# Optimization experiments

Hardware: AMD Instinct MI355X
Metric: run time of the kernel (lower is better)

## Reference

```python
import jax, jax.numpy as jnp
import numpy as np

B, T, D, H, L, FF, V = 32, 64, 512, 8, 4, 2048, 128
HD = D // H
TEMP = 0.1
SCALE_BASE = 16.0
NEG = -1e9


def setup_inputs() -> dict:
    key = jax.random.key(0)
    cnt = [0]
    def nk():
        cnt[0] += 1
        return jax.random.fold_in(key, cnt[0])
    def rn(shape, s=0.02):
        return jax.random.normal(nk(), shape, dtype=jnp.float32) * s
    inp = {
        "target_tensor": jax.random.randint(nk(), (B, T), 0, V),
        "mol_encoding": jax.random.normal(nk(), (B, D), dtype=jnp.float32),
        "emb": rn((V, D), 1.0),
        "sa_in_w": rn((L, 3 * D, D)), "sa_in_b": jnp.zeros((L, 3 * D), jnp.float32),
        "sa_out_w": rn((L, D, D)), "sa_out_b": jnp.zeros((L, D), jnp.float32),
        "ca_in_w": rn((L, 3 * D, D)), "ca_in_b": jnp.zeros((L, 3 * D), jnp.float32),
        "ca_out_w": rn((L, D, D)), "ca_out_b": jnp.zeros((L, D), jnp.float32),
        "ff_w1": rn((L, FF, D)), "ff_b1": jnp.zeros((L, FF), jnp.float32),
        "ff_w2": rn((L, D, FF)), "ff_b2": jnp.zeros((L, D), jnp.float32),
        "n1_g": jnp.ones((L, D), jnp.float32), "n1_b": jnp.zeros((L, D), jnp.float32),
        "n2_g": jnp.ones((L, D), jnp.float32), "n2_b": jnp.zeros((L, D), jnp.float32),
        "n3_g": jnp.ones((L, D), jnp.float32), "n3_b": jnp.zeros((L, D), jnp.float32),
        "fn_g": jnp.ones((D,), jnp.float32), "fn_b": jnp.zeros((D,), jnp.float32),
        "out_w1": rn((2 * D, D)), "out_b1": jnp.zeros((2 * D,), jnp.float32),
        "out_w2": rn((1024, 2 * D)), "out_b2": jnp.zeros((1024,), jnp.float32),
        "out_w3": rn((V, 1024)), "out_b3": jnp.zeros((V,), jnp.float32),
    }
    return inp


def _ln(x, g, b, eps=1e-5):
    mu = x.mean(-1, keepdims=True)
    var = ((x - mu) ** 2).mean(-1, keepdims=True)
    return (x - mu) * jax.lax.rsqrt(var + eps) * g + b


def _xpos(x):
    # x: [B, T, D]; XPOS rotary with scale_base=16, downscale=False
    t, d = x.shape[1], x.shape[2]
    half = d // 2
    sv = (jnp.arange(0, d, 2, dtype=jnp.float32) + 0.4 * d) / (1.4 * d)      # [half]
    pos = jnp.arange(t, dtype=jnp.float32)
    scale = sv[None, :] ** (pos / SCALE_BASE)[:, None]                       # [t, half]
    inv_freq = 1.0 / (10000.0 ** (jnp.arange(half, dtype=jnp.float32) / half))
    ang = pos[:, None] * inv_freq[None, :]                                   # [t, half]
    sin = jnp.repeat(jnp.sin(ang) * scale, 2, axis=-1)                       # duplicate_interleave
    cos = jnp.repeat(jnp.cos(ang) * scale, 2, axis=-1)
    x1, x2 = x[..., ::2], x[..., 1::2]
    rot = jnp.stack((-x2, x1), axis=-1).reshape(x.shape)                     # rotate_every_two
    return x * cos + rot * sin


def _mha(q_in, k_in, v_in, in_w, in_b, out_w, out_b, mask):
    wq, wk, wv = jnp.split(in_w, 3, axis=0)
    bq, bk, bv = jnp.split(in_b, 3, axis=0)
    Bq, Tq = q_in.shape[0], q_in.shape[1]
    q = (q_in @ wq.T + bq).reshape(Bq, Tq, H, HD)
    k = (k_in @ wk.T + bk).reshape(Bq, -1, H, HD)
    v = (v_in @ wv.T + bv).reshape(Bq, -1, H, HD)
    scores = jnp.einsum('bqhd,bkhd->bhqk', q, k) / np.float32(np.sqrt(HD))
    if mask is not None:
        scores = jnp.where(mask, NEG, scores)
    p = jax.nn.softmax(scores, axis=-1)
    o = jnp.einsum('bhqk,bkhd->bqhd', p, v).reshape(Bq, Tq, D)
    return o @ out_w.T + out_b


def reference(target_tensor, mol_encoding, emb, sa_in_w, sa_in_b, sa_out_w, sa_out_b,
              ca_in_w, ca_in_b, ca_out_w, ca_out_b, ff_w1, ff_b1, ff_w2, ff_b2,
              n1_g, n1_b, n2_g, n2_b, n3_g, n3_b, fn_g, fn_b,
              out_w1, out_b1, out_w2, out_b2, out_w3, out_b3):
    memory = mol_encoding[:, None, :]                      # [B, 1, D]
    causal = jnp.triu(jnp.ones((T, T), bool), 1)
    samp_key = jax.random.key(1)

    def logits_at(pred, t):
        x = _xpos(emb[pred])                               # [B, T, D]
        mask = causal[None, None] | (pred == 0)[:, None, None, :]
        for i in range(L):
            a = _mha(x, x, x, sa_in_w[i], sa_in_b[i], sa_out_w[i], sa_out_b[i], mask)
            x = _ln(x + a, n1_g[i], n1_b[i])
            c = _mha(x, memory, memory, ca_in_w[i], ca_in_b[i], ca_out_w[i], ca_out_b[i], None)
            x = _ln(x + c, n2_g[i], n2_b[i])
            f = jax.nn.silu(x @ ff_w1[i].T + ff_b1[i]) @ ff_w2[i].T + ff_b2[i]
            x = _ln(x + f, n3_g[i], n3_b[i])
        x = _ln(x, fn_g, fn_b)
        h = jnp.take(x, t - 1, axis=1)                     # [B, D]
        h = jax.nn.gelu(h @ out_w1.T + out_b1, approximate=False)
        h = jax.nn.gelu(h @ out_w2.T + out_b2, approximate=False)
        return h @ out_w3.T + out_b3                       # [B, V]

    def step(pred, t):
        logits = logits_at(pred, t)
        lp = jax.nn.log_softmax(logits / TEMP, axis=-1)
        u = jax.random.uniform(jax.random.fold_in(samp_key, t), lp.shape)
        g = -jnp.log(-jnp.log(u + 1e-9) + 1e-9)
        tok = jnp.argmax(lp + g, axis=-1).astype(jnp.int32)
        return pred.at[:, t].set(tok), logits

    pred0 = jnp.zeros((B, T), jnp.int32).at[:, 0].set(1)
    pred, _ = jax.lax.scan(jax.checkpoint(step), pred0, jnp.arange(1, T))
    return pred
```

## Files before the change

kernel.cpp:

```cpp
#include <hip/hip_runtime.h>
#include <stdint.h>
#include <stddef.h>

#define BB 32
#define TT 64
#define DD 512
#define HH 8
#define HDIM 64
#define LL 4
#define FFD 2048
#define VV 128

#define NBLK 256
#define NTHR 512

__host__ __device__ inline uint32_t rotl32(uint32_t v, int n){ return (v << n) | (v >> (32 - n)); }

__host__ __device__ inline void tf2x32(uint32_t k0, uint32_t k1, uint32_t x0, uint32_t x1,
                                       uint32_t* o0, uint32_t* o1){
  uint32_t ks2 = k0 ^ k1 ^ 0x1BD11BDAu;
  x0 += k0; x1 += k1;
  x0 += x1; x1 = rotl32(x1,13); x1 ^= x0;
  x0 += x1; x1 = rotl32(x1,15); x1 ^= x0;
  x0 += x1; x1 = rotl32(x1,26); x1 ^= x0;
  x0 += x1; x1 = rotl32(x1, 6); x1 ^= x0;
  x0 += k1; x1 += ks2 + 1u;
  x0 += x1; x1 = rotl32(x1,17); x1 ^= x0;
  x0 += x1; x1 = rotl32(x1,29); x1 ^= x0;
  x0 += x1; x1 = rotl32(x1,16); x1 ^= x0;
  x0 += x1; x1 = rotl32(x1,24); x1 ^= x0;
  x0 += ks2; x1 += k0 + 2u;
  x0 += x1; x1 = rotl32(x1,13); x1 ^= x0;
  x0 += x1; x1 = rotl32(x1,15); x1 ^= x0;
  x0 += x1; x1 = rotl32(x1,26); x1 ^= x0;
  x0 += x1; x1 = rotl32(x1, 6); x1 ^= x0;
  x0 += k0; x1 += k1 + 3u;
  x0 += x1; x1 = rotl32(x1,17); x1 ^= x0;
  x0 += x1; x1 = rotl32(x1,29); x1 ^= x0;
  x0 += x1; x1 = rotl32(x1,16); x1 ^= x0;
  x0 += x1; x1 = rotl32(x1,24); x1 ^= x0;
  x0 += k1; x1 += ks2 + 4u;
  x0 += x1; x1 = rotl32(x1,13); x1 ^= x0;
  x0 += x1; x1 = rotl32(x1,15); x1 ^= x0;
  x0 += x1; x1 = rotl32(x1,26); x1 ^= x0;
  x0 += x1; x1 = rotl32(x1, 6); x1 ^= x0;
  x0 += ks2; x1 += k0 + 5u;
  *o0 = x0; *o1 = x1;
}

__device__ inline float dot_f4(const float* __restrict__ a, const float* __restrict__ w, int K){
  float acc = 0.f;
  const float4* a4 = (const float4*)a;
  const float4* w4 = (const float4*)w;
  int K4 = K >> 2;
  for (int k = 0; k < K4; ++k){
    float4 av = a4[k], wv = w4[k];
    acc = fmaf(av.x, wv.x, acc);
    acc = fmaf(av.y, wv.y, acc);
    acc = fmaf(av.z, wv.z, acc);
    acc = fmaf(av.w, wv.w, acc);
  }
  return acc;
}

__device__ inline float block_ln(float v, float g, float bb, float* red){
  __syncthreads();
  float s = v;
  #pragma unroll
  for (int off = 32; off; off >>= 1) s += __shfl_xor(s, off);
  if ((threadIdx.x & 63) == 0) red[threadIdx.x >> 6] = s;
  __syncthreads();
  float mu = (red[0]+red[1]+red[2]+red[3]+red[4]+red[5]+red[6]+red[7]) * (1.0f/512.0f);
  float dv = v - mu;
  float sq = dv * dv;
  #pragma unroll
  for (int off = 32; off; off >>= 1) sq += __shfl_xor(sq, off);
  __syncthreads();
  if ((threadIdx.x & 63) == 0) red[threadIdx.x >> 6] = sq;
  __syncthreads();
  float var = (red[0]+red[1]+red[2]+red[3]+red[4]+red[5]+red[6]+red[7]) * (1.0f/512.0f);
  return dv * (1.0f / sqrtf(var + 1e-5f)) * g + bb;
}

__device__ inline float row_reduce(float v, int wid, int j, float* wred){
  #pragma unroll
  for (int off = 32; off; off >>= 1) v += __shfl_xor(v, off);
  if ((threadIdx.x & 63) == 0) wred[wid] = v;
  __syncthreads();
  float r = wred[2*j] + wred[2*j+1];
  __syncthreads();
  return r;
}

__device__ __forceinline__ void gbar(unsigned* bar, int g){
  __syncthreads();
  if (threadIdx.x == 0){
    unsigned* cnt = bar + g*64;
    unsigned* gen = bar + g*64 + 16;
    __builtin_amdgcn_fence(__ATOMIC_RELEASE, "agent");
    unsigned old = __hip_atomic_load(gen, __ATOMIC_RELAXED, __HIP_MEMORY_SCOPE_AGENT);
    if (__hip_atomic_fetch_add(cnt, 1u, __ATOMIC_RELAXED, __HIP_MEMORY_SCOPE_AGENT) == 31u){
      __hip_atomic_store(cnt, 0u, __ATOMIC_RELAXED, __HIP_MEMORY_SCOPE_AGENT);
      __hip_atomic_fetch_add(gen, 1u, __ATOMIC_RELEASE, __HIP_MEMORY_SCOPE_AGENT);
    } else {
      while (__hip_atomic_load(gen, __ATOMIC_RELAXED, __HIP_MEMORY_SCOPE_AGENT) == old)
        __builtin_amdgcn_s_sleep(1);
    }
    __builtin_amdgcn_fence(__ATOMIC_ACQUIRE, "agent");
  }
  __syncthreads();
}

__global__ void k_tables(float* __restrict__ cosb, float* __restrict__ sinb){
  int tid = blockIdx.x * blockDim.x + threadIdx.x;
  int p = tid >> 8, i = tid & 255;
  float sv = (2.0f * (float)i + 204.8f) / 716.8f;
  float scale = powf(sv, (float)p / 16.0f);
  float invf = 1.0f / powf(10000.0f, (float)i / 256.0f);
  float ang = (float)p * invf;
  cosb[tid] = cosf(ang) * scale;
  sinb[tid] = sinf(ang) * scale;
}

__global__ void k_ca1(const float* __restrict__ mol, const float* __restrict__ w,
                      const float* __restrict__ bias, float* __restrict__ tmp){
  int tid = blockIdx.x * blockDim.x + threadIdx.x;
  int l = tid >> 14; int r = tid & 16383; int b = r >> 9; int d = r & 511;
  const float* wr = w + (size_t)l*3*DD*DD + (size_t)(2*DD + d)*DD;
  tmp[tid] = bias[l*3*DD + 2*DD + d] + dot_f4(mol + (size_t)b*DD, wr, DD);
}

__global__ void k_ca2(const float* __restrict__ tmp, const float* __restrict__ w,
                      const float* __restrict__ bias, float* __restrict__ cac){
  int tid = blockIdx.x * blockDim.x + threadIdx.x;
  int l = tid >> 14; int r = tid & 16383; int b = r >> 9; int d = r & 511;
  const float* wr = w + (size_t)l*DD*DD + (size_t)d*DD;
  cac[tid] = bias[l*DD + d] + dot_f4(tmp + ((size_t)l*BB + b)*DD, wr, DD);
}

__global__ void k_binit(unsigned* __restrict__ bar, int* __restrict__ pred){
  int tid = threadIdx.x;
  bar[tid] = 0u;
  pred[tid]        = ((tid & (TT-1)) == 0) ? 1 : 0;
  pred[tid + 1024] = (((tid + 1024) & (TT-1)) == 0) ? 1 : 0;
}

__global__ void k_pack32(const float* __restrict__ in, float* __restrict__ out,
                         int N, int K, int total){
  int tid = blockIdx.x * blockDim.x + threadIdx.x;
  if (tid >= total) return;
  int S = N * K;
  int l = tid / S, r = tid - l*S;
  int k32 = r / (32*N);
  int r2 = r - k32*32*N;
  int n = r2 >> 5, ku = r2 & 31;
  out[tid] = in[(size_t)l*S + (size_t)n*K + k32*32 + ku];
}

#define CELL4(WARR, KOFF)                                                     \
  _Pragma("unroll")                                                           \
  for (int q = 0; q < 8; ++q){                                                \
    float4 w = WARR[q];                                                       \
    const int kk = (KOFF) + q*4;                                              \
    float4 xa = *(const float4*)&sxp[0*512 + kk];                             \
    float4 xb = *(const float4*)&sxp[1*512 + kk];                             \
    float4 xc = *(const float4*)&sxp[2*512 + kk];                             \
    float4 xd = *(const float4*)&sxp[3*512 + kk];                             \
    a0=fmaf(w.x,xa.x,a0); a0=fmaf(w.y,xa.y,a0); a0=fmaf(w.z,xa.z,a0); a0=fmaf(w.w,xa.w,a0); \
    a1=fmaf(w.x,xb.x,a1); a1=fmaf(w.y,xb.y,a1); a1=fmaf(w.z,xb.z,a1); a1=fmaf(w.w,xb.w,a1); \
    a2=fmaf(w.x,xc.x,a2); a2=fmaf(w.y,xc.y,a2); a2=fmaf(w.z,xc.z,a2); a2=fmaf(w.w,xc.w,a2); \
    a3=fmaf(w.x,xd.x,a3); a3=fmaf(w.y,xd.y,a3); a3=fmaf(w.z,xd.z,a3); a3=fmaf(w.w,xd.w,a3); \
  }

struct KParams {
  const float *emb, *sab, *sob, *f1b, *f2b;
  const float *g1,*b1,*g2,*b2,*g3,*b3,*fg,*fb;
  const float *o1b,*o2b,*o3w,*o3b;
  const float *cosb,*sinb,*cac;
  const float *sawP,*sowP,*f1wP,*f2wP,*o1wP,*o2wP;
  float *kc,*vc,*xl,*qb,*at,*ao,*x2,*fo,*h1,*xf,*hh1,*hh2,*ps3;
  int *pred;
  unsigned *bar;
};

__global__ __launch_bounds__(NTHR) void k_persist(KParams P){
  const int bid = blockIdx.x, tid = threadIdx.x;
  const int g = bid & 7;
  const int m = bid >> 3;
  const int wid = tid >> 6, lane = tid & 63;
  __shared__ __align__(16) float smem[8704];

  for (int t = 1; t < TT; ++t){
    const int pp = t - 1;

    for (int l = 0; l < LL; ++l){
      {
        float* sx   = smem;
        float* part = smem + 2048;
        float* srow = smem + 4096;
        const int j = tid >> 7, d4 = (tid & 127) * 4;
        const int rb = g*4 + j;
        if (l == 0){
          int tok = P.pred[rb*TT + pp];
          #pragma unroll
          for (int e = d4; e < d4 + 4; e += 2){
            int i = e >> 1;
            float c = P.cosb[pp*256 + i], s = P.sinb[pp*256 + i];
            float e0 = P.emb[(size_t)tok*DD + e];
            float e1 = P.emb[(size_t)tok*DD + e + 1];
            sx[j*512 + e]     = fmaf(e0, c, -(e1*s));
            sx[j*512 + e + 1] = fmaf(e1, c, e0*s);
          }
        } else {
          if (tid < 4){
            float a = 0.f, bq = 0.f;
            const float* pr = P.ps3 + (size_t)(g*4 + tid)*64;
            for (int s = 0; s < 32; ++s){ a += pr[s*2]; bq += pr[s*2+1]; }
            float mu = a * (1.0f/512.0f);
            float var = bq * (1.0f/512.0f) - mu*mu;
            srow[tid*2]   = mu;
            srow[tid*2+1] = 1.0f / sqrtf(var + 1e-5f);
          }
          __syncthreads();
          float mu = srow[j*2], rs = srow[j*2+1];
          float4 xv = *(const float4*)&P.x2[(size_t)rb*DD + d4];
          float4 fv = *(const float4*)&P.fo[(size_t)rb*DD + d4];
          const float* g3r = P.g3 + (size_t)(l-1)*DD;
          const float* b3r = P.b3 + (size_t)(l-1)*DD;
          float yv[4] = {xv.x+fv.x, xv.y+fv.y, xv.z+fv.z, xv.w+fv.w};
          #pragma unroll
          for (int i = 0; i < 4; ++i)
            sx[j*512 + d4 + i] = (yv[i]-mu)*rs*g3r[d4+i] + b3r[d4+i];
        }
        __syncthreads();
        if (m == 0){
          float4 v = *(float4*)&sx[j*512 + d4];
          *(float4*)&P.xl[(size_t)rb*DD + d4] = v;
        }
        if (m < 24){
          const int n0 = m*64;
          const float4* wb0 = (const float4*)P.sawP + ((size_t)l*16 + wid*2)*(1536*8)
                            + (size_t)(n0 + lane)*8;
          const float4* wb1 = wb0 + 1536*8;
          float4 w0[8], w1[8];
          #pragma unroll
          for (int q = 0; q < 8; ++q) w0[q] = wb0[q];
          #pragma unroll
          for (int q = 0; q < 8; ++q) w1[q] = wb1[q];
          float a0=0.f,a1=0.f,a2=0.f,a3=0.f;
          const float* sxp = sx;
          const int kb = wid*64;
          CELL4(w0, kb);
          CELL4(w1, kb + 32);
          part[(wid*4+0)*64 + lane] = a0;
          part[(wid*4+1)*64 + lane] = a1;
          part[(wid*4+2)*64 + lane] = a2;
          part[(wid*4+3)*64 + lane] = a3;
          __syncthreads();
          if (tid < 256){
            int jr = tid >> 6, nl = tid & 63;
            int n = n0 + nl, rb2 = g*4 + jr;
            float s = P.sab[l*1536 + n];
            #pragma unroll
            for (int w = 0; w < 8; ++w) s += part[(w*4+jr)*64 + nl];
            if (n < DD){
              P.qb[(size_t)rb2*DD + n] = s;
            } else if (n < 2*DD){
              int h = (n - DD) >> 6, hd = (n - DD) & 63;
              P.kc[((((size_t)l*BB + rb2)*HH + h)*TT + pp)*HDIM + hd] = s;
            } else {
              int h = (n - 2*DD) >> 6, hd = (n - 2*DD) & 63;
              P.vc[((((size_t)l*BB + rb2)*HH + h)*TT + pp)*HDIM + hd] = s;
            }
          }
        }
      }
      gbar(P.bar, g);

      {
        int bl = m >> 3, h = m & 7, rb = g*4 + bl;
        float* qs = smem; float* ps = smem + 64;
        if (tid < 64) qs[tid] = P.qb[(size_t)rb*DD + h*HDIM + tid];
        __syncthreads();
        if (tid < 64){
          const float* kb = P.kc + (((size_t)l*BB + rb)*HH + h)*TT*HDIM;
          float s = -INFINITY;
          if (lane <= pp && P.pred[rb*TT + lane] != 0){
            const float* kr = kb + lane*HDIM;
            float acc = 0.f;
            #pragma unroll
            for (int k2 = 0; k2 < HDIM; ++k2) acc = fmaf(qs[k2], kr[k2], acc);
            s = acc * 0.125f;
          }
          float mx = s;
          #pragma unroll
          for (int off = 32; off; off >>= 1) mx = fmaxf(mx, __shfl_xor(mx, off));
          float e = (s == -INFINITY) ? 0.f : expf(s - mx);
          float sum = e;
          #pragma unroll
          for (int off = 32; off; off >>= 1) sum += __shfl_xor(sum, off);
          ps[lane] = e / sum;
          const float* vb = P.vc + (((size_t)l*BB + rb)*HH + h)*TT*HDIM;
          float o = 0.f;
          int jj = 0;
          for (; jj + 8 <= t; jj += 8){
            float vv[8];
            #pragma unroll
            for (int u = 0; u < 8; ++u) vv[u] = vb[(jj+u)*HDIM + lane];
            #pragma unroll
            for (int u = 0; u < 8; ++u) o = fmaf(ps[jj+u], vv[u], o);
          }
          for (; jj <= pp; ++jj) o = fmaf(ps[jj], vb[jj*HDIM + lane], o);
          P.at[(size_t)rb*DD + h*HDIM + lane] = o;
        }
      }
      gbar(P.bar, g);

      {
        float* ats  = smem;
        float* part = smem + 2048;
        const int j = tid >> 7, d4 = (tid & 127) * 4;
        *(float4*)&ats[j*512 + d4] = *(const float4*)&P.at[(size_t)(g*4+j)*DD + d4];
        __syncthreads();
        const int n0 = m*16;
        const int jb = lane >> 4, nc = lane & 15;
        const float4* wb0 = (const float4*)P.sowP + ((size_t)l*16 + wid*2)*(512*8)
                          + (size_t)(n0 + nc)*8;
        const float4* wb1 = wb0 + 512*8;
        float4 w0[8], w1[8];
        #pragma unroll
        for (int q = 0; q < 8; ++q) w0[q] = wb0[q];
        #pragma unroll
        for (int q = 0; q < 8; ++q) w1[q] = wb1[q];
        float acc = 0.f;
        const int kb = wid*64;
        #pragma unroll
        for (int q = 0; q < 8; ++q){
          float4 w = w0[q];
          float4 xa = *(const float4*)&ats[jb*512 + kb + q*4];
          acc=fmaf(w.x,xa.x,acc); acc=fmaf(w.y,xa.y,acc); acc=fmaf(w.z,xa.z,acc); acc=fmaf(w.w,xa.w,acc);
        }
        #pragma unroll
        for (int q = 0; q < 8; ++q){
          float4 w = w1[q];
          float4 xa = *(const float4*)&ats[jb*512 + kb + 32 + q*4];
          acc=fmaf(w.x,xa.x,acc); acc=fmaf(w.y,xa.y,acc); acc=fmaf(w.z,xa.z,acc); acc=fmaf(w.w,xa.w,acc);
        }
        part[wid*64 + lane] = acc;
        __syncthreads();
        if (tid < 64){
          int jb2 = tid >> 4, nc2 = tid & 15, n = n0 + nc2;
          float s = P.sob[l*DD + n];
          #pragma unroll
          for (int w = 0; w < 8; ++w) s += part[w*64 + jb2*16 + nc2];
          P.ao[(size_t)(g*4+jb2)*DD + n] = s;
        }
      }
      gbar(P.bar, g);

      {
        float* sx2  = smem;
        float* part = smem + 2048;
        float* wred = smem + 4096;
        const int j = tid >> 7, d4 = (tid & 127) * 4;
        const int rb = g*4 + j;
        float4 xlv = *(const float4*)&P.xl[(size_t)rb*DD + d4];
        float4 aov = *(const float4*)&P.ao[(size_t)rb*DD + d4];
        float y[4] = {xlv.x+aov.x, xlv.y+aov.y, xlv.z+aov.z, xlv.w+aov.w};
        float s = ((y[0]+y[1])+y[2])+y[3];
        float mu = row_reduce(s, wid, j, wred) * (1.0f/512.0f);
        float dv[4], sq = 0.f;
        #pragma unroll
        for (int i = 0; i < 4; ++i){ dv[i] = y[i]-mu; sq += dv[i]*dv[i]; }
        float rs = 1.0f / sqrtf(row_reduce(sq, wid, j, wred) * (1.0f/512.0f) + 1e-5f);
        float z[4];
        #pragma unroll
        for (int i = 0; i < 4; ++i){
          int d = d4 + i;
          z[i] = dv[i]*rs*P.g1[l*DD+d] + P.b1[l*DD+d] + P.cac[((size_t)l*BB + rb)*DD + d];
        }
        float s2 = ((z[0]+z[1])+z[2])+z[3];
        float mu2 = row_reduce(s2, wid, j, wred) * (1.0f/512.0f);
        float dz[4], sq2 = 0.f;
        #pragma unroll
        for (int i = 0; i < 4; ++i){ dz[i] = z[i]-mu2; sq2 += dz[i]*dz[i]; }
        float rs2 = 1.0f / sqrtf(row_reduce(sq2, wid, j, wred) * (1.0f/512.0f) + 1e-5f);
        float x2v[4];
        #pragma unroll
        for (int i = 0; i < 4; ++i){
          int d = d4 + i;
          x2v[i] = dz[i]*rs2*P.g2[l*DD+d] + P.b2[l*DD+d];
          sx2[j*512 + d] = x2v[i];
        }
        if (m == 0) *(float4*)&P.x2[(size_t)rb*DD + d4] = make_float4(x2v[0],x2v[1],x2v[2],x2v[3]);
        __syncthreads();
        const int n0 = m*64;
        const float4* wb0 = (const float4*)P.f1wP + ((size_t)l*16 + wid*2)*(2048*8)
                          + (size_t)(n0 + lane)*8;
        const float4* wb1 = wb0 + 2048*8;
        float4 w0[8], w1[8];
        #pragma unroll
        for (int q = 0; q < 8; ++q) w0[q] = wb0[q];
        #pragma unroll
        for (int q = 0; q < 8; ++q) w1[q] = wb1[q];
        float a0=0.f,a1=0.f,a2=0.f,a3=0.f;
        const float* sxp = sx2;
        const int kb = wid*64;
        CELL4(w0, kb);
        CELL4(w1, kb + 32);
        part[(wid*4+0)*64 + lane] = a0;
        part[(wid*4+1)*64 + lane] = a1;
        part[(wid*4+2)*64 + lane] = a2;
        part[(wid*4+3)*64 + lane] = a3;
        __syncthreads();
        if (tid < 256){
          int jr = tid >> 6, nl = tid & 63;
          int n = n0 + nl;
          float v = P.f1b[l*FFD + n];
          #pragma unroll
          for (int w = 0; w < 8; ++w) v += part[(w*4+jr)*64 + nl];
          P.h1[(size_t)(g*4+jr)*FFD + n] = v / (1.0f + expf(-v));
        }
      }
      gbar(P.bar, g);

      {
        float* sh1  = smem;
        float* part = smem + 8192;
        #pragma unroll
        for (int q = 0; q < 4; ++q){
          int fi = tid + q*512;
          int j = fi >> 9, c4 = fi & 511;
          *(float4*)&sh1[j*2048 + c4*4] = *(const float4*)&P.h1[(size_t)(g*4+j)*FFD + c4*4];
        }
        __syncthreads();
        const int n0 = m*16;
        const int jb = lane >> 4, nc = lane & 15;
        const float4* base = (const float4*)P.f2wP + ((size_t)l*64 + wid*8)*(512*8)
                           + (size_t)(n0 + nc)*8;
        float acc = 0.f;
        #pragma unroll
        for (int cc = 0; cc < 4; ++cc){
          const float4* b0 = base + (size_t)(cc*2)*(512*8);
          const float4* b1 = b0 + 512*8;
          float4 w0[8], w1[8];
          #pragma unroll
          for (int q = 0; q < 8; ++q) w0[q] = b0[q];
          #pragma unroll
          for (int q = 0; q < 8; ++q) w1[q] = b1[q];
          const int kb = wid*256 + cc*64;
          #pragma unroll
          for (int q = 0; q < 8; ++q){
            float4 w = w0[q];
            float4 xa = *(const float4*)&sh1[jb*2048 + kb + q*4];
            acc=fmaf(w.x,xa.x,acc); acc=fmaf(w.y,xa.y,acc); acc=fmaf(w.z,xa.z,acc); acc=fmaf(w.w,xa.w,acc);
          }
          #pragma unroll
          for (int q = 0; q < 8; ++q){
            float4 w = w1[q];
            float4 xa = *(const float4*)&sh1[jb*2048 + kb + 32 + q*4];
            acc=fmaf(w.x,xa.x,acc); acc=fmaf(w.y,xa.y,acc); acc=fmaf(w.z,xa.z,acc); acc=fmaf(w.w,xa.w,acc);
          }
        }
        part[wid*64 + lane] = acc;
        __syncthreads();
        if (tid < 64){
          int jb2 = tid >> 4, nc2 = tid & 15, n = n0 + nc2;
          int rb2 = g*4 + jb2;
          float val = P.f2b[l*DD + n];
          #pragma unroll
          for (int w = 0; w < 8; ++w) val += part[w*64 + jb2*16 + nc2];
          P.fo[(size_t)rb2*DD + n] = val;
          float y = P.x2[(size_t)rb2*DD + n] + val;
          float s1 = y, sq = y*y;
          #pragma unroll
          for (int off = 1; off < 16; off <<= 1){
            s1 += __shfl_xor(s1, off);
            sq += __shfl_xor(sq, off);
          }
          if (nc2 == 0){
            P.ps3[(size_t)(rb2*32 + m)*2]     = s1;
            P.ps3[(size_t)(rb2*32 + m)*2 + 1] = sq;
          }
        }
      }
      gbar(P.bar, g);
    }

    if (m < 4){
      int rb = g*4 + m, d = tid;
      float y = P.x2[(size_t)rb*DD + d] + P.fo[(size_t)rb*DD + d];
      float xv = block_ln(y, P.g3[3*DD + d], P.b3[3*DD + d], smem);
      float o  = block_ln(xv, P.fg[d], P.fb[d], smem);
      P.xf[(size_t)rb*DD + d] = o;
    }
    gbar(P.bar, g);

    {
      float* sxf  = smem;
      float* part = smem + 2048;
      const int j = tid >> 7, d4 = (tid & 127) * 4;
      *(float4*)&sxf[j*512 + d4] = *(const float4*)&P.xf[(size_t)(g*4+j)*DD + d4];
      __syncthreads();
      const int n0 = m*32;
      const int jh = lane >> 5, nc = lane & 31;
      const float4* wb0 = (const float4*)P.o1wP + (size_t)(wid*2)*(1024*8)
                        + (size_t)(n0 + nc)*8;
      const float4* wb1 = wb0 + 1024*8;
      float4 w0[8], w1[8];
      #pragma unroll
      for (int q = 0; q < 8; ++q) w0[q] = wb0[q];
      #pragma unroll
      for (int q = 0; q < 8; ++q) w1[q] = wb1[q];
      float ac0 = 0.f, ac1 = 0.f;
      const int kb = wid*64;
      #pragma unroll
      for (int q = 0; q < 8; ++q){
        float4 w = w0[q];
        float4 xa = *(const float4*)&sxf[jh*512 + kb + q*4];
        float4 xb = *(const float4*)&sxf[(jh+2)*512 + kb + q*4];
        ac0=fmaf(w.x,xa.x,ac0); ac0=fmaf(w.y,xa.y,ac0); ac0=fmaf(w.z,xa.z,ac0); ac0=fmaf(w.w,xa.w,ac0);
        ac1=fmaf(w.x,xb.x,ac1); ac1=fmaf(w.y,xb.y,ac1); ac1=fmaf(w.z,xb.z,ac1); ac1=fmaf(w.w,xb.w,ac1);
      }
      #pragma unroll
      for (int q = 0; q < 8; ++q){
        float4 w = w1[q];
        float4 xa = *(const float4*)&sxf[jh*512 + kb + 32 + q*4];
        float4 xb = *(const float4*)&sxf[(jh+2)*512 + kb + 32 + q*4];
        ac0=fmaf(w.x,xa.x,ac0); ac0=fmaf(w.y,xa.y,ac0); ac0=fmaf(w.z,xa.z,ac0); ac0=fmaf(w.w,xa.w,ac0);
        ac1=fmaf(w.x,xb.x,ac1); ac1=fmaf(w.y,xb.y,ac1); ac1=fmaf(w.z,xb.z,ac1); ac1=fmaf(w.w,xb.w,ac1);
      }
      part[(wid*2+0)*64 + lane] = ac0;
      part[(wid*2+1)*64 + lane] = ac1;
      __syncthreads();
      if (tid < 128){
        int row = tid >> 5, nc2 = tid & 31;
        int r = row >> 1, jh2 = row & 1;
        float s = P.o1b[n0 + nc2];
        #pragma unroll
        for (int w = 0; w < 8; ++w) s += part[(w*2+r)*64 + jh2*32 + nc2];
        float a = s;
        P.hh1[(size_t)(g*4+row)*1024 + n0 + nc2] = 0.5f * a * (1.0f + erff(a / 1.41421356237309504880f));
      }
    }
    gbar(P.bar, g);

    {
      float* sh   = smem;
      float* part = smem + 4096;
      #pragma unroll
      for (int q = 0; q < 2; ++q){
        int fi = tid + q*512;
        int j = fi >> 8, c4 = fi & 255;
        *(float4*)&sh[j*1024 + c4*4] = *(const float4*)&P.hh1[(size_t)(g*4+j)*1024 + c4*4];
      }
      __syncthreads();
      const int n0 = m*32;
      const int jh = lane >> 5, nc = lane & 31;
      const float4* base = (const float4*)P.o2wP + (size_t)(wid*4)*(1024*8)
                         + (size_t)(n0 + nc)*8;
      float ac0 = 0.f, ac1 = 0.f;
      #pragma unroll
      for (int cc = 0; cc < 2; ++cc){
        const float4* b0 = base + (size_t)(cc*2)*(1024*8);
        const float4* b1 = b0 + 1024*8;
        float4 w0[8], w1[8];
        #pragma unroll
        for (int q = 0; q < 8; ++q) w0[q] = b0[q];
        #pragma unroll
        for (int q = 0; q < 8; ++q) w1[q] = b1[q];
        const int kb = wid*128 + cc*64;
        #pragma unroll
        for (int q = 0; q < 8; ++q){
          float4 w = w0[q];
          float4 xa = *(const float4*)&sh[jh*1024 + kb + q*4];
          float4 xb = *(const float4*)&sh[(jh+2)*1024 + kb + q*4];
          ac0=fmaf(w.x,xa.x,ac0); ac0=fmaf(w.y,xa.y,ac0); ac0=fmaf(w.z,xa.z,ac0); ac0=fmaf(w.w,xa.w,ac0);
          ac1=fmaf(w.x,xb.x,ac1); ac1=fmaf(w.y,xb.y,ac1); ac1=fmaf(w.z,xb.z,ac1); ac1=fmaf(w.w,xb.w,ac1);
        }
        #pragma unroll
        for (int q = 0; q < 8; ++q){
          float4 w = w1[q];
          float4 xa = *(const float4*)&sh[jh*1024 + kb + 32 + q*4];
          float4 xb = *(const float4*)&sh[(jh+2)*1024 + kb + 32 + q*4];
          ac0=fmaf(w.x,xa.x,ac0); ac0=fmaf(w.y,xa.y,ac0); ac0=fmaf(w.z,xa.z,ac0); ac0=fmaf(w.w,xa.w,ac0);
          ac1=fmaf(w.x,xb.x,ac1); ac1=fmaf(w.y,xb.y,ac1); ac1=fmaf(w.z,xb.z,ac1); ac1=fmaf(w.w,xb.w,ac1);
        }
      }
      part[(wid*2+0)*64 + lane] = ac0;
      part[(wid*2+1)*64 + lane] = ac1;
      __syncthreads();
      if (tid < 128){
        int row = tid >> 5, nc2 = tid & 31;
        int r = row >> 1, jh2 = row & 1;
        float s = P.o2b[n0 + nc2];
        #pragma unroll
        for (int w = 0; w < 8; ++w) s += part[(w*2+r)*64 + jh2*32 + nc2];
        float a = s;
        P.hh2[(size_t)(g*4+row)*1024 + n0 + nc2] = 0.5f * a * (1.0f + erff(a / 1.41421356237309504880f));
      }
    }
    gbar(P.bar, g);

    if (m < 4){
      int rb = g*4 + m, v = tid;
      float* hrow = smem;
      float* red  = smem + 1024;
      int*   redi = (int*)(smem + 1032);
      for (int k = tid; k < 1024; k += NTHR) hrow[k] = P.hh2[(size_t)rb*1024 + k];
      __syncthreads();
      float sv = 0.f;
      if (tid < 128){
        float acc = P.o3b[v] + dot_f4(hrow, P.o3w + (size_t)v*1024, 1024);
        sv = acc / 0.1f;
      }
      float mx = (tid < 128) ? sv : -INFINITY;
      #pragma unroll
      for (int off = 32; off; off >>= 1) mx = fmaxf(mx, __shfl_xor(mx, off));
      __syncthreads();
      if (tid < 128 && (tid & 63) == 0) red[tid >> 6] = mx;
      __syncthreads();
      mx = fmaxf(red[0], red[1]);
      float e = (tid < 128) ? expf(sv - mx) : 0.f;
      float sum = e;
      #pragma unroll
      for (int off = 32; off; off >>= 1) sum += __shfl_xor(sum, off);
      __syncthreads();
      if (tid < 128 && (tid & 63) == 0) red[tid >> 6] = sum;
      __syncthreads();
      sum = red[0] + red[1];
      float bv = -INFINITY; int bi = 0x7fffffff;
      if (tid < 128){
        float lp = (sv - mx) - logf(sum);
        uint32_t kk0, kk1, o0, o1;
        tf2x32(0u, 1u, 0u, (uint32_t)t, &kk0, &kk1);
        tf2x32(kk0, kk1, 0u, (uint32_t)(rb*VV + v), &o0, &o1);
        uint32_t bits = o0 ^ o1;
        float u = __uint_as_float((bits >> 9) | 0x3F800000u) - 1.0f;
        float gg = -logf(-logf(u + 1e-9f) + 1e-9f);
        bv = lp + gg; bi = v;
      }
      #pragma unroll
      for (int off = 32; off; off >>= 1){
        float ov = __shfl_xor(bv, off);
        int   oi = __shfl_xor(bi, off);
        if (ov > bv || (ov == bv && oi < bi)){ bv = ov; bi = oi; }
      }
      __syncthreads();
      if (tid < 128 && (tid & 63) == 0){ red[tid >> 6] = bv; redi[tid >> 6] = bi; }
      __syncthreads();
      if (tid == 0){
        float v0 = red[0], v1 = red[1]; int i0 = redi[0], i1 = redi[1];
        P.pred[rb*TT + t] = (v1 > v0 || (v1 == v0 && i1 < i0)) ? i1 : i0;
      }
    }
    gbar(P.bar, g);
  }
}

extern "C" void kernel_launch(void* const* d_in, const int* in_sizes, int n_in,
                              void* d_out, int out_size, void* d_ws, size_t ws_size,
                              hipStream_t stream){
  (void)in_sizes; (void)n_in; (void)out_size; (void)ws_size;
  const float* mol      = (const float*)d_in[1];
  const float* sa_in_w  = (const float*)d_in[3];
  const float* sa_out_w = (const float*)d_in[5];
  const float* ca_in_w  = (const float*)d_in[7];
  const float* ca_in_b  = (const float*)d_in[8];
  const float* ca_out_w = (const float*)d_in[9];
  const float* ca_out_b = (const float*)d_in[10];
  const float* ff_w1    = (const float*)d_in[11];
  const float* ff_w2    = (const float*)d_in[13];
  const float* out_w1   = (const float*)d_in[23];
  const float* out_w2   = (const float*)d_in[25];

  KParams P;
  P.emb = (const float*)d_in[2];
  P.sab = (const float*)d_in[4];
  P.sob = (const float*)d_in[6];
  P.f1b = (const float*)d_in[12];
  P.f2b = (const float*)d_in[14];
  P.g1  = (const float*)d_in[15];
  P.b1  = (const float*)d_in[16];
  P.g2  = (const float*)d_in[17];
  P.b2  = (const float*)d_in[18];
  P.g3  = (const float*)d_in[19];
  P.b3  = (const float*)d_in[20];
  P.fg  = (const float*)d_in[21];
  P.fb  = (const float*)d_in[22];
  P.o1b = (const float*)d_in[24];
  P.o2b = (const float*)d_in[26];
  P.o3w = (const float*)d_in[27];
  P.o3b = (const float*)d_in[28];

  unsigned* bar = (unsigned*)d_ws;
  float* ws = (float*)d_ws + 1024;
  float* cosb   = ws;
  float* sinb   = cosb + 16384;
  float* ca_tmp = sinb + 16384;
  float* cac    = ca_tmp + 65536;
  float* kc     = cac + 65536;
  float* vc     = kc + 4194304;
  float* xl     = vc + 4194304;
  float* qb     = xl + 16384;
  float* at     = qb + 16384;
  float* ao     = at + 16384;
  float* x2     = ao + 16384;
  float* fo     = x2 + 16384;
  float* h1     = fo + 16384;
  float* xf     = h1 + 65536;
  float* hh1    = xf + 16384;
  float* hh2    = hh1 + 32768;
  float* ps3    = hh2 + 32768;
  float* sawP   = ps3 + 2048;
  float* sowP   = sawP + 3145728;
  float* f1wP   = sowP + 1048576;
  float* f2wP   = f1wP + 4194304;
  float* o1wP   = f2wP + 4194304;
  float* o2wP   = o1wP + 524288;

  P.cosb = cosb; P.sinb = sinb; P.cac = cac;
  P.kc = kc; P.vc = vc; P.xl = xl; P.qb = qb; P.at = at; P.ao = ao;
  P.x2 = x2; P.fo = fo; P.h1 = h1; P.xf = xf; P.hh1 = hh1; P.hh2 = hh2;
  P.ps3 = ps3;
  P.sawP = sawP; P.sowP = sowP; P.f1wP = f1wP; P.f2wP = f2wP;
  P.o1wP = o1wP; P.o2wP = o2wP;
  P.pred = (int*)d_out;
  P.bar = bar;

  k_binit<<<1, 1024, 0, stream>>>(bar, P.pred);
  k_tables<<<64, 256, 0, stream>>>(cosb, sinb);
  k_ca1<<<256, 256, 0, stream>>>(mol, ca_in_w, ca_in_b, ca_tmp);
  k_ca2<<<256, 256, 0, stream>>>(ca_tmp, ca_out_w, ca_out_b, cac);

  {
    int t1 = 4*1536*512;  k_pack32<<<(t1+255)/256, 256, 0, stream>>>(sa_in_w,  sawP, 1536, 512,  t1);
    int t2 = 4*512*512;   k_pack32<<<(t2+255)/256, 256, 0, stream>>>(sa_out_w, sowP,  512, 512,  t2);
    int t3 = 4*2048*512;  k_pack32<<<(t3+255)/256, 256, 0, stream>>>(ff_w1,    f1wP, 2048, 512,  t3);
    int t4 = 4*512*2048;  k_pack32<<<(t4+255)/256, 256, 0, stream>>>(ff_w2,    f2wP,  512, 2048, t4);
    int t5 = 1024*512;    k_pack32<<<(t5+255)/256, 256, 0, stream>>>(out_w1,   o1wP, 1024, 512,  t5);
    int t6 = 1024*1024;   k_pack32<<<(t6+255)/256, 256, 0, stream>>>(out_w2,   o2wP, 1024, 1024, t6);
  }

  k_persist<<<NBLK, NTHR, 0, stream>>>(P);
}
```

Before: 23.45 ms.

## Double persistent blocks to 512 and split GEMV stages into finer column tiles

Raises the persistent grid from 256 to 512 blocks, so each group barrier now counts 64 blocks, and requests 4 blocks per CU through launch bounds. The matrix-vector stages (QKV, out-proj, FF1, output heads) are re-tiled so each block computes half as many output columns, spreading weight streaming across more CUs; attention and FF2 stages only use the first 32 blocks per group. This adds barrier participants and idle blocks in some stages in exchange for more memory-level parallelism in the weight-bound stages.

```diff
diff --git a/kernel.cpp b/kernel.cpp
--- a/kernel.cpp
+++ b/kernel.cpp
@@ -11,7 +11,7 @@
 #define FFD 2048
 #define VV 128
 
-#define NBLK 256
+#define NBLK 512
 #define NTHR 512
 
 __host__ __device__ inline uint32_t rotl32(uint32_t v, int n){ return (v << n) | (v >> (32 - n)); }
@@ -99,7 +99,7 @@
     unsigned* gen = bar + g*64 + 16;
     __builtin_amdgcn_fence(__ATOMIC_RELEASE, "agent");
     unsigned old = __hip_atomic_load(gen, __ATOMIC_RELAXED, __HIP_MEMORY_SCOPE_AGENT);
-    if (__hip_atomic_fetch_add(cnt, 1u, __ATOMIC_RELAXED, __HIP_MEMORY_SCOPE_AGENT) == 31u){
+    if (__hip_atomic_fetch_add(cnt, 1u, __ATOMIC_RELAXED, __HIP_MEMORY_SCOPE_AGENT) == 63u){
       __hip_atomic_store(cnt, 0u, __ATOMIC_RELAXED, __HIP_MEMORY_SCOPE_AGENT);
       __hip_atomic_fetch_add(gen, 1u, __ATOMIC_RELEASE, __HIP_MEMORY_SCOPE_AGENT);
     } else {
@@ -157,19 +157,15 @@
   out[tid] = in[(size_t)l*S + (size_t)n*K + k32*32 + ku];
 }
 
-#define CELL4(WARR, KOFF)                                                     \
+#define CELL2(WARR, KOFF, J0)                                                 \
   _Pragma("unroll")                                                           \
   for (int q = 0; q < 8; ++q){                                                \
     float4 w = WARR[q];                                                       \
     const int kk = (KOFF) + q*4;                                              \
-    float4 xa = *(const float4*)&sxp[0*512 + kk];                             \
-    float4 xb = *(const float4*)&sxp[1*512 + kk];                             \
-    float4 xc = *(const float4*)&sxp[2*512 + kk];                             \
-    float4 xd = *(const float4*)&sxp[3*512 + kk];                             \
-    a0=fmaf(w.x,xa.x,a0); a0=fmaf(w.y,xa.y,a0); a0=fmaf(w.z,xa.z,a0); a0=fmaf(w.w,xa.w,a0); \
-    a1=fmaf(w.x,xb.x,a1); a1=fmaf(w.y,xb.y,a1); a1=fmaf(w.z,xb.z,a1); a1=fmaf(w.w,xb.w,a1); \
-    a2=fmaf(w.x,xc.x,a2); a2=fmaf(w.y,xc.y,a2); a2=fmaf(w.z,xc.z,a2); a2=fmaf(w.w,xc.w,a2); \
-    a3=fmaf(w.x,xd.x,a3); a3=fmaf(w.y,xd.y,a3); a3=fmaf(w.z,xd.z,a3); a3=fmaf(w.w,xd.w,a3); \
+    float4 xa = *(const float4*)&sxp[(J0)*512 + kk];                          \
+    float4 xb = *(const float4*)&sxp[((J0)+1)*512 + kk];                      \
+    r0=fmaf(w.x,xa.x,r0); r0=fmaf(w.y,xa.y,r0); r0=fmaf(w.z,xa.z,r0); r0=fmaf(w.w,xa.w,r0); \
+    r1=fmaf(w.x,xb.x,r1); r1=fmaf(w.y,xb.y,r1); r1=fmaf(w.z,xb.z,r1); r1=fmaf(w.w,xb.w,r1); \
   }
 
 struct KParams {
@@ -183,7 +179,7 @@
   unsigned *bar;
 };
 
-__global__ __launch_bounds__(NTHR) void k_persist(KParams P){
+__global__ __launch_bounds__(NTHR, 4) void k_persist(KParams P){
   const int bid = blockIdx.x, tid = threadIdx.x;
   const int g = bid & 7;
   const int m = bid >> 3;
@@ -237,32 +233,31 @@
           float4 v = *(float4*)&sx[j*512 + d4];
           *(float4*)&P.xl[(size_t)rb*DD + d4] = v;
         }
-        if (m < 24){
-          const int n0 = m*64;
+        if (m < 48){
+          const int n0 = m*32;
+          const int c = lane & 31, j0 = (lane >> 5) * 2;
           const float4* wb0 = (const float4*)P.sawP + ((size_t)l*16 + wid*2)*(1536*8)
-                            + (size_t)(n0 + lane)*8;
+                            + (size_t)(n0 + c)*8;
           const float4* wb1 = wb0 + 1536*8;
           float4 w0[8], w1[8];
           #pragma unroll
           for (int q = 0; q < 8; ++q) w0[q] = wb0[q];
           #pragma unroll
           for (int q = 0; q < 8; ++q) w1[q] = wb1[q];
-          float a0=0.f,a1=0.f,a2=0.f,a3=0.f;
+          float r0=0.f, r1=0.f;
           const float* sxp = sx;
           const int kb = wid*64;
-          CELL4(w0, kb);
-          CELL4(w1, kb + 32);
-          part[(wid*4+0)*64 + lane] = a0;
-          part[(wid*4+1)*64 + lane] = a1;
-          part[(wid*4+2)*64 + lane] = a2;
-          part[(wid*4+3)*64 + lane] = a3;
+          CELL2(w0, kb, j0);
+          CELL2(w1, kb + 32, j0);
+          part[(wid*4 + j0)*32 + c]     = r0;
+          part[(wid*4 + j0 + 1)*32 + c] = r1;
           __syncthreads();
-          if (tid < 256){
-            int jr = tid >> 6, nl = tid & 63;
+          if (tid < 128){
+            int jr = tid >> 5, nl = tid & 31;
             int n = n0 + nl, rb2 = g*4 + jr;
             float s = P.sab[l*1536 + n];
             #pragma unroll
-            for (int w = 0; w < 8; ++w) s += part[(w*4+jr)*64 + nl];
+            for (int w = 0; w < 8; ++w) s += part[(w*4+jr)*32 + nl];
             if (n < DD){
               P.qb[(size_t)rb2*DD + n] = s;
             } else if (n < 2*DD){
@@ -277,7 +272,7 @@
       }
       gbar(P.bar, g);
 
-      {
+      if (m < 32){
         int bl = m >> 3, h = m & 7, rb = g*4 + bl;
         float* qs = smem; float* ps = smem + 64;
         if (tid < 64) qs[tid] = P.qb[(size_t)rb*DD + h*HDIM + tid];
@@ -322,37 +317,39 @@
         const int j = tid >> 7, d4 = (tid & 127) * 4;
         *(float4*)&ats[j*512 + d4] = *(const float4*)&P.at[(size_t)(g*4+j)*DD + d4];
         __syncthreads();
-        const int n0 = m*16;
-        const int jb = lane >> 4, nc = lane & 15;
-        const float4* wb0 = (const float4*)P.sowP + ((size_t)l*16 + wid*2)*(512*8)
-                          + (size_t)(n0 + nc)*8;
-        const float4* wb1 = wb0 + 512*8;
-        float4 w0[8], w1[8];
-        #pragma unroll
-        for (int q = 0; q < 8; ++q) w0[q] = wb0[q];
-        #pragma unroll
-        for (int q = 0; q < 8; ++q) w1[q] = wb1[q];
-        float acc = 0.f;
-        const int kb = wid*64;
-        #pragma unroll
-        for (int q = 0; q < 8; ++q){
-          float4 w = w0[q];
-          float4 xa = *(const float4*)&ats[jb*512 + kb + q*4];
-          acc=fmaf(w.x,xa.x,acc); acc=fmaf(w.y,xa.y,acc); acc=fmaf(w.z,xa.z,acc); acc=fmaf(w.w,xa.w,acc);
-        }
-        #pragma unroll
-        for (int q = 0; q < 8; ++q){
-          float4 w = w1[q];
-          float4 xa = *(const float4*)&ats[jb*512 + kb + 32 + q*4];
-          acc=fmaf(w.x,xa.x,acc); acc=fmaf(w.y,xa.y,acc); acc=fmaf(w.z,xa.z,acc); acc=fmaf(w.w,xa.w,acc);
-        }
-        part[wid*64 + lane] = acc;
+        const int n0 = m*8;
+        if (lane < 32){
+          int jb = lane >> 3, nc = lane & 7;
+          const float4* wb0 = (const float4*)P.sowP + ((size_t)l*16 + wid*2)*(512*8)
+                            + (size_t)(n0 + nc)*8;
+          const float4* wb1 = wb0 + 512*8;
+          float4 w0[8], w1[8];
+          #pragma unroll
+          for (int q = 0; q < 8; ++q) w0[q] = wb0[q];
+          #pragma unroll
+          for (int q = 0; q < 8; ++q) w1[q] = wb1[q];
+          float acc = 0.f;
+          const int kb = wid*64;
+          #pragma unroll
+          for (int q = 0; q < 8; ++q){
+            float4 w = w0[q];
+            float4 xa = *(const float4*)&ats[jb*512 + kb + q*4];
+            acc=fmaf(w.x,xa.x,acc); acc=fmaf(w.y,xa.y,acc); acc=fmaf(w.z,xa.z,acc); acc=fmaf(w.w,xa.w,acc);
+          }
+          #pragma unroll
+          for (int q = 0; q < 8; ++q){
+            float4 w = w1[q];
+            float4 xa = *(const float4*)&ats[jb*512 + kb + 32 + q*4];
+            acc=fmaf(w.x,xa.x,acc); acc=fmaf(w.y,xa.y,acc); acc=fmaf(w.z,xa.z,acc); acc=fmaf(w.w,xa.w,acc);
+          }
+          part[wid*32 + jb*8 + nc] = acc;
+        }
         __syncthreads();
-        if (tid < 64){
-          int jb2 = tid >> 4, nc2 = tid & 15, n = n0 + nc2;
+        if (tid < 32){
+          int jb2 = tid >> 3, nc2 = tid & 7, n = n0 + nc2;
           float s = P.sob[l*DD + n];
           #pragma unroll
-          for (int w = 0; w < 8; ++w) s += part[w*64 + jb2*16 + nc2];
+          for (int w = 0; w < 8; ++w) s += part[w*32 + jb2*8 + nc2];
           P.ao[(size_t)(g*4+jb2)*DD + n] = s;
         }
       }
@@ -394,37 +391,36 @@
         }
         if (m == 0) *(float4*)&P.x2[(size_t)rb*DD + d4] = make_float4(x2v[0],x2v[1],x2v[2],x2v[3]);
         __syncthreads();
-        const int n0 = m*64;
+        const int n0 = m*32;
+        const int c = lane & 31, j0 = (lane >> 5) * 2;
         const float4* wb0 = (const float4*)P.f1wP + ((size_t)l*16 + wid*2)*(2048*8)
-                          + (size_t)(n0 + lane)*8;
+                          + (size_t)(n0 + c)*8;
         const float4* wb1 = wb0 + 2048*8;
         float4 w0[8], w1[8];
         #pragma unroll
         for (int q = 0; q < 8; ++q) w0[q] = wb0[q];
         #pragma unroll
         for (int q = 0; q < 8; ++q) w1[q] = wb1[q];
-        float a0=0.f,a1=0.f,a2=0.f,a3=0.f;
+        float r0=0.f, r1=0.f;
         const float* sxp = sx2;
         const int kb = wid*64;
-        CELL4(w0, kb);
-        CELL4(w1, kb + 32);
-        part[(wid*4+0)*64 + lane] = a0;
-        part[(wid*4+1)*64 + lane] = a1;
-        part[(wid*4+2)*64 + lane] = a2;
-        part[(wid*4+3)*64 + lane] = a3;
+        CELL2(w0, kb, j0);
+        CELL2(w1, kb + 32, j0);
+        part[(wid*4 + j0)*32 + c]     = r0;
+        part[(wid*4 + j0 + 1)*32 + c] = r1;
         __syncthreads();
-        if (tid < 256){
-          int jr = tid >> 6, nl = tid & 63;
+        if (tid < 128){
+          int jr = tid >> 5, nl = tid & 31;
           int n = n0 + nl;
           float v = P.f1b[l*FFD + n];
           #pragma unroll
-          for (int w = 0; w < 8; ++w) v += part[(w*4+jr)*64 + nl];
+          for (int w = 0; w < 8; ++w) v += part[(w*4+jr)*32 + nl];
           P.h1[(size_t)(g*4+jr)*FFD + n] = v / (1.0f + expf(-v));
         }
       }
       gbar(P.bar, g);
 
-      {
+      if (m < 32){
         float* sh1  = smem;
         float* part = smem + 8192;
         #pragma unroll
@@ -502,45 +498,38 @@
       const int j = tid >> 7, d4 = (tid & 127) * 4;
       *(float4*)&sxf[j*512 + d4] = *(const float4*)&P.xf[(size_t)(g*4+j)*DD + d4];
       __syncthreads();
-      const int n0 = m*32;
-      const int jh = lane >> 5, nc = lane & 31;
+      const int n0 = m*16;
+      const int row = lane >> 4, col = lane & 15;
       const float4* wb0 = (const float4*)P.o1wP + (size_t)(wid*2)*(1024*8)
-                        + (size_t)(n0 + nc)*8;
+                        + (size_t)(n0 + col)*8;
       const float4* wb1 = wb0 + 1024*8;
       float4 w0[8], w1[8];
       #pragma unroll
       for (int q = 0; q < 8; ++q) w0[q] = wb0[q];
       #pragma unroll
       for (int q = 0; q < 8; ++q) w1[q] = wb1[q];
-      float ac0 = 0.f, ac1 = 0.f;
+      float acc = 0.f;
       const int kb = wid*64;
       #pragma unroll
       for (int q = 0; q < 8; ++q){
         float4 w = w0[q];
-        float4 xa = *(const float4*)&sxf[jh*512 + kb + q*4];
-        float4 xb = *(const float4*)&sxf[(jh+2)*512 + kb + q*4];
-        ac0=fmaf(w.x,xa.x,ac0); ac0=fmaf(w.y,xa.y,ac0); ac0=fmaf(w.z,xa.z,ac0); ac0=fmaf(w.w,xa.w,ac0);
-        ac1=fmaf(w.x,xb.x,ac1); ac1=fmaf(w.y,xb.y,ac1); ac1=fmaf(w.z,xb.z,ac1); ac1=fmaf(w.w,xb.w,ac1);
+        float4 xa = *(const float4*)&sxf[row*512 + kb + q*4];
+        acc=fmaf(w.x,xa.x,acc); acc=fmaf(w.y,xa.y,acc); acc=fmaf(w.z,xa.z,acc); acc=fmaf(w.w,xa.w,acc);
       }
       #pragma unroll
       for (int q = 0; q < 8; ++q){
         float4 w = w1[q];
-        float4 xa = *(const float4*)&sxf[jh*512 + kb + 32 + q*4];
-        float4 xb = *(const float4*)&sxf[(jh+2)*512 + kb + 32 + q*4];
-        ac0=fmaf(w.x,xa.x,ac0); ac0=fmaf(w.y,xa.y,ac0); ac0=fmaf(w.z,xa.z,ac0); ac0=fmaf(w.w,xa.w,ac0);
-        ac1=fmaf(w.x,xb.x,ac1); ac1=fmaf(w.y,xb.y,ac1); ac1=fmaf(w.z,xb.z,ac1); ac1=fmaf(w.w,xb.w,ac1);
-      }
-      part[(wid*2+0)*64 + lane] = ac0;
-      part[(wid*2+1)*64 + lane] = ac1;
-      __syncthreads();
-      if (tid < 128){
-        int row = tid >> 5, nc2 = tid & 31;
-        int r = row >> 1, jh2 = row & 1;
-        float s = P.o1b[n0 + nc2];
-        #pragma unroll
-        for (int w = 0; w < 8; ++w) s += part[(w*2+r)*64 + jh2*32 + nc2];
-        float a = s;
-        P.hh1[(size_t)(g*4+row)*1024 + n0 + nc2] = 0.5f * a * (1.0f + erff(a / 1.41421356237309504880f));
+        float4 xa = *(const float4*)&sxf[row*512 + kb + 32 + q*4];
+        acc=fmaf(w.x,xa.x,acc); acc=fmaf(w.y,xa.y,acc); acc=fmaf(w.z,xa.z,acc); acc=fmaf(w.w,xa.w,acc);
+      }
+      part[wid*64 + row*16 + col] = acc;
+      __syncthreads();
+      if (tid < 64){
+        int row2 = tid >> 4, col2 = tid & 15, n = n0 + col2;
+        float a = P.o1b[n];
+        #pragma unroll
+        for (int w = 0; w < 8; ++w) a += part[w*64 + row2*16 + col2];
+        P.hh1[(size_t)(g*4+row2)*1024 + n] = 0.5f * a * (1.0f + erff(a / 1.41421356237309504880f));
       }
     }
     gbar(P.bar, g);
@@ -555,11 +544,11 @@
         *(float4*)&sh[j*1024 + c4*4] = *(const float4*)&P.hh1[(size_t)(g*4+j)*1024 + c4*4];
       }
       __syncthreads();
-      const int n0 = m*32;
-      const int jh = lane >> 5, nc = lane & 31;
+      const int n0 = m*16;
+      const int row = lane >> 4, col = lane & 15;
       const float4* base = (const float4*)P.o2wP + (size_t)(wid*4)*(1024*8)
-                         + (size_t)(n0 + nc)*8;
-      float ac0 = 0.f, ac1 = 0.f;
+                         + (size_t)(n0 + col)*8;
+      float acc = 0.f;
       #pragma unroll
       for (int cc = 0; cc < 2; ++cc){
         const float4* b0 = base + (size_t)(cc*2)*(1024*8);
@@ -573,31 +562,24 @@
         #pragma unroll
         for (int q = 0; q < 8; ++q){
           float4 w = w0[q];
-          float4 xa = *(const float4*)&sh[jh*1024 + kb + q*4];
-          float4 xb = *(const float4*)&sh[(jh+2)*1024 + kb + q*4];
-          ac0=fmaf(w.x,xa.x,ac0); ac0=fmaf(w.y,xa.y,ac0); ac0=fmaf(w.z,xa.z,ac0); ac0=fmaf(w.w,xa.w,ac0);
-          ac1=fmaf(w.x,xb.x,ac1); ac1=fmaf(w.y,xb.y,ac1); ac1=fmaf(w.z,xb.z,ac1); ac1=fmaf(w.w,xb.w,ac1);
+          float4 xa = *(const float4*)&sh[row*1024 + kb + q*4];
+          acc=fmaf(w.x,xa.x,acc); acc=fmaf(w.y,xa.y,acc); acc=fmaf(w.z,xa.z,acc); acc=fmaf(w.w,xa.w,acc);
         }
         #pragma unroll
         for (int q = 0; q < 8; ++q){
           float4 w = w1[q];
-          float4 xa = *(const float4*)&sh[jh*1024 + kb + 32 + q*4];
-          float4 xb = *(const float4*)&sh[(jh+2)*1024 + kb + 32 + q*4];
-          ac0=fmaf(w.x,xa.x,ac0); ac0=fmaf(w.y,xa.y,ac0); ac0=fmaf(w.z,xa.z,ac0); ac0=fmaf(w.w,xa.w,ac0);
-          ac1=fmaf(w.x,xb.x,ac1); ac1=fmaf(w.y,xb.y,ac1); ac1=fmaf(w.z,xb.z,ac1); ac1=fmaf(w.w,xb.w,ac1);
-        }
-      }
-      part[(wid*2+0)*64 + lane] = ac0;
-      part[(wid*2+1)*64 + lane] = ac1;
-      __syncthreads();
-      if (tid < 128){
-        int row = tid >> 5, nc2 = tid & 31;
-        int r = row >> 1, jh2 = row & 1;
-        float s = P.o2b[n0 + nc2];
-        #pragma unroll
-        for (int w = 0; w < 8; ++w) s += part[(w*2+r)*64 + jh2*32 + nc2];
-        float a = s;
-        P.hh2[(size_t)(g*4+row)*1024 + n0 + nc2] = 0.5f * a * (1.0f + erff(a / 1.41421356237309504880f));
+          float4 xa = *(const float4*)&sh[row*1024 + kb + 32 + q*4];
+          acc=fmaf(w.x,xa.x,acc); acc=fmaf(w.y,xa.y,acc); acc=fmaf(w.z,xa.z,acc); acc=fmaf(w.w,xa.w,acc);
+        }
+      }
+      part[wid*64 + row*16 + col] = acc;
+      __syncthreads();
+      if (tid < 64){
+        int row2 = tid >> 4, col2 = tid & 15, n = n0 + col2;
+        float a = P.o2b[n];
+        #pragma unroll
+        for (int w = 0; w < 8; ++w) a += part[w*64 + row2*16 + col2];
+        P.hh2[(size_t)(g*4+row2)*1024 + n] = 0.5f * a * (1.0f + erff(a / 1.41421356237309504880f));
       }
     }
     gbar(P.bar, g);
@@ -607,6 +589,7 @@
       float* hrow = smem;
       float* red  = smem + 1024;
       int*   redi = (int*)(smem + 1032);
+      int*   stok = (int*)(smem + 1040);
       for (int k = tid; k < 1024; k += NTHR) hrow[k] = P.hh2[(size_t)rb*1024 + k];
       __syncthreads();
       float sv = 0.f;
@@ -651,8 +634,11 @@
       __syncthreads();
       if (tid == 0){
         float v0 = red[0], v1 = red[1]; int i0 = redi[0], i1 = redi[1];
-        P.pred[rb*TT + t] = (v1 > v0 || (v1 == v0 && i1 < i0)) ? i1 : i0;
-      }
+        int tok = (v1 > v0 || (v1 == v0 && i1 < i0)) ? i1 : i0;
+        P.pred[rb*TT + t] = tok;
+        *stok = tok;
+      }
+      __syncthreads();
     }
     gbar(P.bar, g);
   }
```

Result: slower. 41.84 ms (+78.4%).
